# Kernel optimization log

Hardware: AMD Instinct MI355X
Metric: run time of the kernel (lower is better)

The kernel has to match this reference:

```python
import jax, jax.numpy as jnp
import numpy as np

E, H = 256, 4
DH = E // H                      # head dim 64
DHALF, N, R, K = 256, 16, 16, 5  # mamba d_inner//2, d_state, dt_rank, d_conv
B, L = 2, 2048


def _ln(x, g, b):
    m = jnp.mean(x, -1, keepdims=True)
    v = jnp.var(x, -1, keepdims=True)
    return (x - m) * jax.lax.rsqrt(v + 1e-5) * g + b


def _rotate_half(x):
    y = x.reshape(x.shape[:-1] + (-1, 2))
    return jnp.stack((-y[..., 1], y[..., 0]), -1).reshape(x.shape)


def _dwconv(x, w):  # x: (B,C,L), w: (C,1,K), depthwise 'same' conv, no bias (conv_bias//2 == 0)
    return jax.lax.conv_general_dilated(
        x, w, (1,), 'SAME', feature_group_count=x.shape[1],
        dimension_numbers=('NCH', 'OIH', 'NCH'))


def _selective_scan(x, dt, A_log, Bm, Cm, Dp, dt_bias):
    # x, dt: (B,Dh,L); Bm, Cm: (B,N,L); A_log: (Dh,N); Dp, dt_bias: (Dh,)
    A = -jnp.exp(A_log)
    delta = jax.nn.softplus(dt + dt_bias[None, :, None])
    seq = (jnp.moveaxis(delta, 2, 0), jnp.moveaxis(x, 2, 0),
           jnp.moveaxis(Bm, 2, 0), jnp.moveaxis(Cm, 2, 0))
    h0 = jnp.zeros((x.shape[0], A.shape[0], A.shape[1]), x.dtype)

    def step(h, inp):
        d_l, x_l, B_l, C_l = inp
        h = jnp.exp(d_l[:, :, None] * A) * h + (d_l * x_l)[:, :, None] * B_l[:, None, :]
        return h, jnp.einsum('bdn,bn->bd', h, C_l)

    _, ys = jax.lax.scan(step, h0, seq)
    return jnp.moveaxis(ys, 0, 2) + Dp[None, :, None] * x


def _forward(desc0, desc1, pe0, pe1, qkv_w, qkv_b, attn_out_w, attn_out_b,
             ma_ffn_w1, ma_ffn_b1, ma_ffn_g, ma_ffn_beta, ma_ffn_w2, ma_ffn_b2,
             m_in_w, m_convx_w, m_convz_w, m_xproj_w, m_dt_w, m_dt_b, m_Alog, m_D, m_out_w,
             ca_qk_w, ca_qk_b, ca_v_w, ca_v_b, ca_out_w, ca_out_b,
             ca_ffn_w1, ca_ffn_b1, ca_ffn_g, ca_ffn_beta, ca_ffn_w2, ca_ffn_b2):

    def mamba_twopath(x_in):
        xz = jnp.swapaxes(x_in @ m_in_w.T, 1, 2)           # (B, 2*Dh, L)
        xc, zc = xz[:, :DHALF], xz[:, DHALF:]
        xc = jax.nn.silu(_dwconv(xc, m_convx_w))
        zc = jax.nn.silu(_dwconv(zc, m_convz_w))
        x_dbl = jnp.einsum('bdl,kd->bkl', xc, m_xproj_w)   # (B, R+2N, L)
        # dt_proj applies its bias here AND the same bias is re-added inside the scan
        # (delta_bias), exactly as in the torch source.
        dt = jnp.einsum('brl,dr->bdl', x_dbl[:, :R], m_dt_w) + m_dt_b[None, :, None]
        Bm, Cm = x_dbl[:, R:R + N], x_dbl[:, R + N:]
        y = _selective_scan(xc, dt, m_Alog, Bm, Cm, m_D, m_dt_b)  # (B, Dh, L)
        return jnp.swapaxes(y, 1, 2) @ m_out_w.T, jnp.swapaxes(zc, 1, 2) @ m_out_w.T

    def ma_ffn(h):
        h = _ln(h @ ma_ffn_w1.T + ma_ffn_b1, ma_ffn_g, ma_ffn_beta)
        return jax.nn.gelu(h, approximate=False) @ ma_ffn_w2.T + ma_ffn_b2

    def mamba_attention(x, pe):
        b, l, _ = x.shape
        qkv = (x @ qkv_w.T + qkv_b).reshape(b, l, H, DH, 3)
        qkv = jnp.swapaxes(qkv, 1, 2)                       # (B,H,L,DH,3)
        q, k, v = qkv[..., 0], qkv[..., 1], qkv[..., 2]
        q = q * pe[0] + _rotate_half(q) * pe[1]
        k = k * pe[0] + _rotate_half(k) * pe[1]
        attn = jax.nn.softmax(jnp.einsum('bhid,bhjd->bhij', q, k) * DH ** -0.5, -1)
        o = jnp.einsum('bhij,bhjd->bhid', attn, v)
        o = jnp.swapaxes(o, 1, 2).reshape(b, l, E) @ attn_out_w.T + attn_out_b
        s_x, c_x = mamba_twopath(x)
        return x + ma_ffn(jnp.concatenate([x, o, s_x, c_x], -1))

    def ca_ffn(h):
        h = _ln(h @ ca_ffn_w1.T + ca_ffn_b1, ca_ffn_g, ca_ffn_beta)
        return jax.nn.gelu(h, approximate=False) @ ca_ffn_w2.T + ca_ffn_b2

    def split_heads(t):
        b, l, _ = t.shape
        return jnp.swapaxes(t.reshape(b, l, H, DH), 1, 2)

    def cross_attn(x0, x1):
        s = DH ** -0.25  # scale**0.5 applied to both qk0 and qk1
        qk0 = split_heads(x0 @ ca_qk_w.T + ca_qk_b) * s
        qk1 = split_heads(x1 @ ca_qk_w.T + ca_qk_b) * s
        v0 = split_heads(x0 @ ca_v_w.T + ca_v_b)
        v1 = split_heads(x1 @ ca_v_w.T + ca_v_b)
        sim = jnp.einsum('bhid,bhjd->bhij', qk0, qk1)       # (B,H,L0,L1)
        m0 = jnp.einsum('bhij,bhjd->bhid', jax.nn.softmax(sim, -1), v1)
        m1 = jnp.einsum('bhji,bhjd->bhid', jax.nn.softmax(sim, -2), v0)
        b, l = x0.shape[0], x0.shape[1]
        m0 = jnp.swapaxes(m0, 1, 2).reshape(b, l, E) @ ca_out_w.T + ca_out_b
        m1 = jnp.swapaxes(m1, 1, 2).reshape(b, x1.shape[1], E) @ ca_out_w.T + ca_out_b
        x0 = x0 + ca_ffn(jnp.concatenate([x0, m0], -1))
        x1 = x1 + ca_ffn(jnp.concatenate([x1, m1], -1))
        return x0, x1

    d0 = mamba_attention(desc0, pe0)
    d1 = mamba_attention(desc1, pe1)
    return cross_attn(d0, d1)


def setup_inputs():
    key = jax.random.key(0)
    ks = jax.random.split(key, 32)
    rn = lambda i, shape, s=0.02: jax.random.normal(ks[i], shape, jnp.float32) * s
    rng = np.random.default_rng(0)
    dt = np.exp(rng.uniform(size=DHALF) * (np.log(0.1) - np.log(0.001)) + np.log(0.001))
    inv_dt = dt + np.log(-np.expm1(-dt))
    return {
        'desc0': jax.random.normal(ks[0], (B, L, E), jnp.float32),
        'desc1': jax.random.normal(ks[1], (B, L, E), jnp.float32),
        'pe0': jax.random.normal(ks[2], (2, B, 1, L, DH), jnp.float32),
        'pe1': jax.random.normal(ks[3], (2, B, 1, L, DH), jnp.float32),
        'qkv_w': rn(4, (3 * E, E)), 'qkv_b': rn(5, (3 * E,)),
        'attn_out_w': rn(6, (E, E)), 'attn_out_b': rn(7, (E,)),
        'ma_ffn_w1': rn(8, (2 * E, 4 * E)), 'ma_ffn_b1': rn(9, (2 * E,)),
        'ma_ffn_g': jnp.ones((2 * E,), jnp.float32), 'ma_ffn_beta': jnp.zeros((2 * E,), jnp.float32),
        'ma_ffn_w2': rn(10, (E, 2 * E)), 'ma_ffn_b2': rn(11, (E,)),
        'm_in_w': rn(12, (2 * DHALF, E)),
        'm_convx_w': rn(13, (DHALF, 1, K), 0.2), 'm_convz_w': rn(14, (DHALF, 1, K), 0.2),
        'm_xproj_w': rn(15, (R + 2 * N, DHALF)),
        'm_dt_w': rn(16, (DHALF, R), R ** -0.5),
        'm_dt_b': jnp.asarray(inv_dt, jnp.float32),
        'm_Alog': jnp.log(jnp.broadcast_to(jnp.arange(1, N + 1, dtype=jnp.float32), (DHALF, N))),
        'm_D': jnp.ones((DHALF,), jnp.float32),
        'm_out_w': rn(17, (E, DHALF)),
        'ca_qk_w': rn(18, (E, E)), 'ca_qk_b': rn(19, (E,)),
        'ca_v_w': rn(20, (E, E)), 'ca_v_b': rn(21, (E,)),
        'ca_out_w': rn(22, (E, E)), 'ca_out_b': rn(23, (E,)),
        'ca_ffn_w1': rn(24, (2 * E, 2 * E)), 'ca_ffn_b1': rn(25, (2 * E,)),
        'ca_ffn_g': jnp.ones((2 * E,), jnp.float32), 'ca_ffn_beta': jnp.zeros((2 * E,), jnp.float32),
        'ca_ffn_w2': rn(26, (E, 2 * E)), 'ca_ffn_b2': rn(27, (E,)),
    }


def reference(desc0, desc1, pe0, pe1, qkv_w, qkv_b, attn_out_w, attn_out_b,
              ma_ffn_w1, ma_ffn_b1, ma_ffn_g, ma_ffn_beta, ma_ffn_w2, ma_ffn_b2,
              m_in_w, m_convx_w, m_convz_w, m_xproj_w, m_dt_w, m_dt_b, m_Alog, m_D, m_out_w,
              ca_qk_w, ca_qk_b, ca_v_w, ca_v_b, ca_out_w, ca_out_b,
              ca_ffn_w1, ca_ffn_b1, ca_ffn_g, ca_ffn_beta, ca_ffn_w2, ca_ffn_b2):
    return _forward(desc0, desc1, pe0, pe1, qkv_w, qkv_b, attn_out_w, attn_out_b,
                    ma_ffn_w1, ma_ffn_b1, ma_ffn_g, ma_ffn_beta, ma_ffn_w2, ma_ffn_b2,
                    m_in_w, m_convx_w, m_convz_w, m_xproj_w, m_dt_w, m_dt_b, m_Alog, m_D, m_out_w,
                    ca_qk_w, ca_qk_b, ca_v_w, ca_v_b, ca_out_w, ca_out_b,
                    ca_ffn_w1, ca_ffn_b1, ca_ffn_g, ca_ffn_beta, ca_ffn_w2, ca_ffn_b2)
```

## Files before the change

### kernel.cpp

```cpp
#include <hip/hip_runtime.h>

typedef unsigned short u16;
typedef short s16;
typedef s16 s16x8 __attribute__((ext_vector_type(8)));
typedef float f32x4 __attribute__((ext_vector_type(4)));

__device__ __forceinline__ float bf2f(u16 u){
  union { unsigned int i; float f; } v; v.i = ((unsigned int)u) << 16; return v.f;
}
__device__ __forceinline__ u16 f2bf(float f){
  union { float f; unsigned int u; } v; v.f = f;
  unsigned int r = (v.u + 0x7fffu + ((v.u >> 16) & 1u)) >> 16;
  return (u16)r;
}
__device__ __forceinline__ unsigned int cvtpk(float lo, float hi){
  unsigned int d;
  asm("v_cvt_pk_bf16_f32 %0, %1, %2" : "=v"(d) : "v"(lo), "v"(hi));
  return d;
}
__device__ __forceinline__ uint4 pack8(float4 a0, float4 a1){
  uint4 v;
  v.x = cvtpk(a0.x, a0.y); v.y = cvtpk(a0.z, a0.w);
  v.z = cvtpk(a1.x, a1.y); v.w = cvtpk(a1.z, a1.w);
  return v;
}
__device__ __forceinline__ float gelu_f(float x){
  return 0.5f * x * (1.f + erff(x * 0.70710678118654752440f));
}
__device__ __forceinline__ float ldw(const void* p, long i, int fl){
  return fl ? bf2f(((const u16*)p)[i]) : ((const float*)p)[i];
}
__device__ __forceinline__ float4 ldw4(const void* p, long i, int fl){
  if (fl){
    ushort4 w = *(const ushort4*)((const u16*)p + i);
    return make_float4(bf2f(w.x), bf2f(w.y), bf2f(w.z), bf2f(w.w));
  }
  return *(const float4*)((const float*)p + i);
}

template<int C>
__device__ __forceinline__ float dppf(float x){
  return __int_as_float(__builtin_amdgcn_update_dpp(0, __float_as_int(x), C, 0xf, 0xf, true));
}
__device__ __forceinline__ float dppmax16(float v){
  v = fmaxf(v, dppf<0xB1>(v));
  v = fmaxf(v, dppf<0x4E>(v));
  v = fmaxf(v, dppf<0x141>(v));
  v = fmaxf(v, dppf<0x140>(v));
  return v;
}
__device__ __forceinline__ float dppsum16(float v){
  v += dppf<0xB1>(v);
  v += dppf<0x4E>(v);
  v += dppf<0x141>(v);
  v += dppf<0x140>(v);
  return v;
}

__global__ __launch_bounds__(256) void k_sniff(const unsigned int* __restrict__ w,
                                               int n, int* __restrict__ flag){
  __shared__ int cnt[256];
  int c = 0;
  for (int i = threadIdx.x; i < n; i += 256){
    unsigned e = (w[i] >> 7) & 0xFFu;
    c += (e >= 120u && e <= 127u) ? 1 : 0;
  }
  cnt[threadIdx.x] = c; __syncthreads();
  for (int s = 128; s > 0; s >>= 1){
    if (threadIdx.x < s) cnt[threadIdx.x] += cnt[threadIdx.x + s];
    __syncthreads();
  }
  if (threadIdx.x == 0) flag[0] = (2 * cnt[0] > n) ? 1 : 0;
  if (threadIdx.x == 1) flag[1] = 0;
}

__global__ __launch_bounds__(256) void k_pad(
  const void* __restrict__ wx, const void* __restrict__ wd,
  const void* __restrict__ bd,
  float* __restrict__ px, float* __restrict__ pd, float* __restrict__ pb,
  const int* __restrict__ flagp)
{
  int fl = *flagp;
  int i = blockIdx.x * 256 + threadIdx.x;
  if (i < 16384){
    int r = i >> 8, c = i & 255;
    px[i] = (r < 48) ? ldw(wx, r*256 + c, fl) : 0.f;
  } else if (i < 32768){
    int j = i - 16384;
    int n = j >> 6, k = j & 63;
    pd[j] = (k < 16) ? ldw(wd, n*16 + k, fl) : 0.f;
  } else if (i < 33024){
    pb[i - 32768] = ldw(bd, i - 32768, fl);
  }
}

__global__ __launch_bounds__(256) void k_gemm_mfma(
  const void* __restrict__ A, int aflidx, int lda, int K, int N,
  const void* __restrict__ W, const void* __restrict__ W2, int nsplit, int wflidx,
  const void* __restrict__ bias,
  float* __restrict__ Cf, u16* __restrict__ Cb, int ldc,
  float* __restrict__ C2, int ldc2,
  const void* __restrict__ resid, int rflidx, int ldr,
  const void* __restrict__ csrc, int cflidx, float* __restrict__ cdst,
  float oscale, int act_gelu, int outmode, const int* __restrict__ flagp)
{
  const int fl  = flagp[0];
  const int afl = flagp[aflidx];
  const int wfl = flagp[wflidx];
  const int rfl = flagp[rflidx];
  const int cfl = flagp[cflidx];
  __shared__ u16 As[64*72];
  __shared__ u16 Bs[64*72];
  const int tid = threadIdx.x;
  const int w = tid >> 6, lane = tid & 63, quad = lane >> 4, m = lane & 15;
  const int m0 = blockIdx.y << 6, n0 = blockIdx.x << 6;
  const int srow = tid >> 2, sc0 = (tid & 3) << 4;
  const int reg2 = (n0 >= nsplit);
  const void* Wp = reg2 ? W2 : W;
  const int nbase = reg2 ? nsplit : 0;

  f32x4 acc[4];
  #pragma unroll
  for (int ct = 0; ct < 4; ++ct) acc[ct] = (f32x4){0.f,0.f,0.f,0.f};

  for (int k0 = 0; k0 < K; k0 += 64){
    {
      long ab = (long)(m0 + srow) * lda + k0 + sc0;
      if (afl && !act_gelu){
        #pragma unroll
        for (int g = 0; g < 2; ++g)
          *(uint4*)&As[srow*72 + sc0 + g*8] = *(const uint4*)((const u16*)A + ab + g*8);
      } else {
        #pragma unroll
        for (int g = 0; g < 2; ++g){
          float4 a0 = ldw4(A, ab + g*8, afl);
          float4 a1 = ldw4(A, ab + g*8 + 4, afl);
          if (act_gelu){
            a0.x=gelu_f(a0.x); a0.y=gelu_f(a0.y); a0.z=gelu_f(a0.z); a0.w=gelu_f(a0.w);
            a1.x=gelu_f(a1.x); a1.y=gelu_f(a1.y); a1.z=gelu_f(a1.z); a1.w=gelu_f(a1.w);
          }
          *(uint4*)&As[srow*72 + sc0 + g*8] = pack8(a0, a1);
        }
      }
    }
    {
      long wb = (long)(n0 + srow - nbase) * K + k0 + sc0;
      if (wfl){
        #pragma unroll
        for (int g = 0; g < 2; ++g)
          *(uint4*)&Bs[srow*72 + sc0 + g*8] = *(const uint4*)((const u16*)Wp + wb + g*8);
      } else {
        #pragma unroll
        for (int g = 0; g < 2; ++g){
          float4 b0 = *(const float4*)((const float*)Wp + wb + g*8);
          float4 b1 = *(const float4*)((const float*)Wp + wb + g*8 + 4);
          *(uint4*)&Bs[srow*72 + sc0 + g*8] = pack8(b0, b1);
        }
      }
    }
    __syncthreads();

    s16x8 av[2];
    #pragma unroll
    for (int s = 0; s < 2; ++s)
      av[s] = *(const s16x8*)&As[(w*16 + m)*72 + s*32 + quad*8];
    #pragma unroll
    for (int ct = 0; ct < 4; ++ct)
      #pragma unroll
      for (int s = 0; s < 2; ++s){
        s16x8 bv = *(const s16x8*)&Bs[(ct*16 + m)*72 + s*32 + quad*8];
        acc[ct] = __builtin_amdgcn_mfma_f32_16x16x32_bf16(av[s], bv, acc[ct], 0, 0, 0);
      }
    __syncthreads();
  }

  if (outmode == 4){
    const int gmb = m0 + w*16 + quad*4;
    #pragma unroll
    for (int ct = 0; ct < 4; ++ct){
      int gn = n0 + ct*16 + m;
      float bv = ldw(bias, gn, wfl);
      float dl4[4], dx4[4];
      #pragma unroll
      for (int r = 0; r < 4; ++r){
        float dl = acc[ct][r] + bv + bv;
        float delta = (dl > 20.f) ? dl : __logf(1.f + __expf(dl));
        dl4[r] = delta;
        dx4[r] = delta * ldw(resid, (long)(gmb + r) * ldr + gn, rfl);
      }
      *(float4*)&Cf[(long)gn * ldc + gmb] = make_float4(dl4[0], dl4[1], dl4[2], dl4[3]);
      *(float4*)&C2[(long)gn * ldc2 + gmb] = make_float4(dx4[0], dx4[1], dx4[2], dx4[3]);
    }
    return;
  }

  #pragma unroll
  for (int r = 0; r < 4; ++r){
    int gm = m0 + w*16 + quad*4 + r;
    #pragma unroll
    for (int ct = 0; ct < 4; ++ct){
      int gn = n0 + ct*16 + m;
      float v = acc[ct][r];
      if (reg2){
        C2[(long)gm * ldc2 + (gn - nsplit)] = v;
      } else {
        if (bias) v += ldw(bias, gn, wfl);
        v *= oscale;
        if (resid) v += ldw(resid, (long)gm * ldr + gn, rfl);
        long off = (long)gm * ldc + gn;
        if (outmode == 2){
          if (fl) Cb[off] = f2bf(v); else Cf[off] = v;
        } else if (outmode == 3){
          Cb[off] = f2bf(v);
        } else {
          Cf[off] = v;
        }
        if (cdst) cdst[(long)gm * ldc + gn] = ldw(csrc, (long)gm * 256 + gn, cfl);
      }
    }
  }
}

struct GB8 {
  const float* A[8]; const void* W[8]; const void* bias[8];
  float* Cf[8]; u16* Cb[8]; const void* resid[8];
  const void* csrc[8]; float* cdst[8]; float osc[8];
  int cfl[8]; int wkoff[8]; int rfli[8];
  const float* aux[8]; const void* dvec;
};

__global__ __launch_bounds__(256) void k_gemmb(
  GB8 gb, int lda, int K, int N, int ldc, int ldr, int ldwq,
  int act_gelu, int outmode, const int* __restrict__ flagp)
{
  const int fl = flagp[0];
  const int z = blockIdx.z;
  const float* A = gb.A[z]; const void* W = gb.W[z]; const void* bias = gb.bias[z];
  float* Cf = gb.Cf[z]; u16* Cb = gb.Cb[z]; const void* resid = gb.resid[z];
  const void* csrc = gb.csrc[z]; float* cdst = gb.cdst[z];
  const float osc = gb.osc[z];
  const int cfl = flagp[gb.cfl[z]];
  const int rfl = flagp[gb.rfli[z]];
  const int wkoff = gb.wkoff[z];
  const float* aux = gb.aux[z];

  __shared__ u16 As[64*72];
  __shared__ u16 Bs[64*72];
  const int tid = threadIdx.x;
  const int w = tid >> 6, lane = tid & 63, quad = lane >> 4, m = lane & 15;
  const int m0 = blockIdx.y << 6, n0 = blockIdx.x << 6;
  const int srow = tid >> 2, sc0 = (tid & 3) << 4;

  f32x4 acc[4];
  #pragma unroll
  for (int ct = 0; ct < 4; ++ct) acc[ct] = (f32x4){0.f,0.f,0.f,0.f};

  for (int k0 = 0; k0 < K; k0 += 64){
    {
      const float* ar = A + (long)(m0 + srow) * lda + k0 + sc0;
      #pragma unroll
      for (int g = 0; g < 2; ++g){
        float4 a0 = *(const float4*)(ar + g*8);
        float4 a1 = *(const float4*)(ar + g*8 + 4);
        if (aux){
          const float* xr = aux + (long)(m0 + srow) * lda + k0 + sc0;
          float4 x0 = *(const float4*)(xr + g*8);
          float4 x1 = *(const float4*)(xr + g*8 + 4);
          float4 d0 = ldw4(gb.dvec, k0 + sc0 + g*8, fl);
          float4 d1 = ldw4(gb.dvec, k0 + sc0 + g*8 + 4, fl);
          a0.x += d0.x*x0.x; a0.y += d0.y*x0.y; a0.z += d0.z*x0.z; a0.w += d0.w*x0.w;
          a1.x += d1.x*x1.x; a1.y += d1.y*x1.y; a1.z += d1.z*x1.z; a1.w += d1.w*x1.w;
        }
        if (act_gelu){
          a0.x=gelu_f(a0.x); a0.y=gelu_f(a0.y); a0.z=gelu_f(a0.z); a0.w=gelu_f(a0.w);
          a1.x=gelu_f(a1.x); a1.y=gelu_f(a1.y); a1.z=gelu_f(a1.z); a1.w=gelu_f(a1.w);
        }
        *(uint4*)&As[srow*72 + sc0 + g*8] = pack8(a0, a1);
      }
    }
    {
      long wb = (long)(n0 + srow) * ldwq + wkoff + k0 + sc0;
      if (fl){
        #pragma unroll
        for (int g = 0; g < 2; ++g)
          *(uint4*)&Bs[srow*72 + sc0 + g*8] = *(const uint4*)((const u16*)W + wb + g*8);
      } else {
        #pragma unroll
        for (int g = 0; g < 2; ++g){
          float4 b0 = *(const float4*)((const float*)W + wb + g*8);
          float4 b1 = *(const float4*)((const float*)W + wb + g*8 + 4);
          *(uint4*)&Bs[srow*72 + sc0 + g*8] = pack8(b0, b1);
        }
      }
    }
    __syncthreads();

    s16x8 av[2];
    #pragma unroll
    for (int s = 0; s < 2; ++s)
      av[s] = *(const s16x8*)&As[(w*16 + m)*72 + s*32 + quad*8];
    #pragma unroll
    for (int ct = 0; ct < 4; ++ct)
      #pragma unroll
      for (int s = 0; s < 2; ++s){
        s16x8 bv = *(const s16x8*)&Bs[(ct*16 + m)*72 + s*32 + quad*8];
        acc[ct] = __builtin_amdgcn_mfma_f32_16x16x32_bf16(av[s], bv, acc[ct], 0, 0, 0);
      }
    __syncthreads();
  }

  #pragma unroll
  for (int r = 0; r < 4; ++r){
    int gm = m0 + w*16 + quad*4 + r;
    #pragma unroll
    for (int ct = 0; ct < 4; ++ct){
      int gn = n0 + ct*16 + m;
      float v = acc[ct][r];
      if (bias) v += ldw(bias, gn, fl);
      v *= osc;
      if (resid) v += ldw(resid, (long)gm * ldr + gn, rfl);
      long off = (long)gm * ldc + gn;
      if (outmode == 2){
        if (fl) Cb[off] = f2bf(v); else Cf[off] = v;
      } else if (outmode == 3){
        Cb[off] = f2bf(v);
      } else {
        Cf[off] = v;
      }
      if (cdst) cdst[(long)gm * ldc + gn] = ldw(csrc, (long)gm * 256 + gn, cfl);
    }
  }
}

__global__ __launch_bounds__(256) void k_rope(
  const float* __restrict__ qkv0, const float* __restrict__ qkv1,
  const void* __restrict__ pe0, const void* __restrict__ pe1,
  u16* __restrict__ q, u16* __restrict__ k, u16* __restrict__ v,
  int L, int B, int H, const int* __restrict__ flagp)
{
  int fl = *flagp;
  int tid = threadIdx.x;
  int lq = tid >> 6, d = tid & 63;
  int l = blockIdx.x * 4 + lq;
  int bh = blockIdx.y;
  int dsc = bh >> 3;
  int bh7 = bh & 7;
  int b = bh7 >> 2, h = bh7 & 3;
  const float* qkv = dsc ? qkv1 : qkv0;
  const void* pe = dsc ? pe1 : pe0;
  const float* row = qkv + ((long)b * L + l) * 768 + h * 192;
  float qv = row[d*3+0], kv = row[d*3+1], vv = row[d*3+2];
  int dn = (d & 1) ? (d - 1) : (d + 1);
  float qn = row[dn*3+0], kn = row[dn*3+1];
  float rq = (d & 1) ? qn : -qn;
  float rk = (d & 1) ? kn : -kn;
  long peo = ((long)b * L + l) * 64 + d;
  float p0 = ldw(pe, peo, fl);
  float p1 = ldw(pe, (long)B * L * 64 + peo, fl);
  long o = ((long)bh * L + l) * 64 + d;
  q[o] = f2bf((qv * p0 + rq * p1) * 0.125f);
  k[o] = f2bf(kv * p0 + rk * p1);
  v[o] = f2bf(vv);
}

__global__ __launch_bounds__(256, 8) void k_attn_mfma(
  const u16* __restrict__ Q, long qsb, long qsh, long qsl,
  const u16* __restrict__ Kp, long ksb, long ksh, long ksl,
  const u16* __restrict__ Vp, long vsb, long vsh, long vsl,
  float* __restrict__ Opart, float* __restrict__ mpart, float* __restrict__ lpart,
  int L, int H, int kchunk)
{
  __shared__ u16 Kt[64*72];
  __shared__ u16 Vt[64*72];
  __shared__ u16 Ps[64*72];
  const int tid  = threadIdx.x;
  const int w    = tid >> 6;
  const int lane = tid & 63;
  const int quad = lane >> 4;
  const int m    = lane & 15;
  const int bh = blockIdx.y, b = bh / H, h = bh % H;
  const int iq0 = blockIdx.x * 64;
  const int z = blockIdx.z;
  const long BHL = (long)gridDim.y * L;

  const u16* Qb = Q  + b*qsb + h*qsh;
  const u16* Kb = Kp + b*ksb + h*ksh;
  const u16* Vb = Vp + b*vsb + h*vsh;

  s16x8 aq[2];
  {
    const u16* qr = Qb + (long)(iq0 + w*16 + m) * qsl + quad*8;
    aq[0] = *(const s16x8*)(qr);
    aq[1] = *(const s16x8*)(qr + 32);
  }

  f32x4 o_acc[4];
  #pragma unroll
  for (int nt = 0; nt < 4; ++nt) o_acc[nt] = (f32x4){0.f,0.f,0.f,0.f};
  float mrow[4] = {-1e30f,-1e30f,-1e30f,-1e30f};
  float lrow[4] = {0.f,0.f,0.f,0.f};

  const int srow = tid >> 2, sc0 = (tid & 3) << 4;
  const int kg = tid & 15;
  const int dg = tid >> 4;
  const int vcb = ((((dg >> 2) * 2) + (kg >> 1)) & 7) * 8 + (kg & 1) * 4;
  const int modd = m & 1;
  const int pcolb = m & 6;
  const int jend = z * kchunk + kchunk;

  for (int j0 = z * kchunk; j0 < jend; j0 += 64){
    {
      const u16* kr = Kb + (long)(j0 + srow) * ksl + sc0;
      *(uint4*)&Kt[srow*72 + sc0]     = *(const uint4*)kr;
      *(uint4*)&Kt[srow*72 + sc0 + 8] = *(const uint4*)(kr + 8);
      const u16* vr = Vb + (long)(j0 + 4*kg) * vsl + 4*dg;
      ushort4 r0 = *(const ushort4*)(vr);
      ushort4 r1 = *(const ushort4*)(vr + vsl);
      ushort4 r2 = *(const ushort4*)(vr + 2*vsl);
      ushort4 r3 = *(const ushort4*)(vr + 3*vsl);
      u16* vt = &Vt[(4*dg)*72 + vcb];
      *(ushort4*)(vt)       = make_ushort4(r0.x, r1.x, r2.x, r3.x);
      *(ushort4*)(vt + 72)  = make_ushort4(r0.y, r1.y, r2.y, r3.y);
      *(ushort4*)(vt + 144) = make_ushort4(r0.z, r1.z, r2.z, r3.z);
      *(ushort4*)(vt + 216) = make_ushort4(r0.w, r1.w, r2.w, r3.w);
    }
    __syncthreads();

    float sv[4][4];
    #pragma unroll
    for (int ct = 0; ct < 4; ++ct){
      f32x4 acc = (f32x4){0.f,0.f,0.f,0.f};
      #pragma unroll
      for (int s = 0; s < 2; ++s){
        s16x8 bk = *(const s16x8*)&Kt[(ct*16 + m)*72 + s*32 + quad*8];
        acc = __builtin_amdgcn_mfma_f32_16x16x32_bf16(aq[s], bk, acc, 0, 0, 0);
      }
      #pragma unroll
      for (int r = 0; r < 4; ++r) sv[ct][r] = acc[r];
    }

    float v0s[4];
    int need = 0;
    #pragma unroll
    for (int r = 0; r < 4; ++r){
      float v0 = fmaxf(fmaxf(sv[0][r], sv[1][r]), fmaxf(sv[2][r], sv[3][r]));
      v0 = dppmax16(v0);
      v0s[r] = v0;
      need |= (v0 > mrow[r] + 8.f) ? 1 : 0;
    }
    if (__any(need)){
      float alpha[4];
      #pragma unroll
      for (int r = 0; r < 4; ++r){
        float mn = fmaxf(mrow[r], v0s[r]);
        alpha[r] = __expf(mrow[r] - mn);
        mrow[r] = mn;
        lrow[r] *= alpha[r];
      }
      #pragma unroll
      for (int nt = 0; nt < 4; ++nt)
        #pragma unroll
        for (int r = 0; r < 4; ++r) o_acc[nt][r] *= alpha[r];
    }
    float rsum[4] = {0.f,0.f,0.f,0.f};
    #pragma unroll
    for (int ct = 0; ct < 4; ++ct)
      #pragma unroll
      for (int r = 0; r < 4; ++r){
        float p = __expf(sv[ct][r] - mrow[r]);
        sv[ct][r] = p;
        rsum[r] += p;
      }
    #pragma unroll
    for (int r = 0; r < 4; ++r)
      lrow[r] += dppsum16(rsum[r]);

    #pragma unroll
    for (int ct = 0; ct < 4; ++ct){
      const int kb = (2*w + 2*ct + (m >> 3)) & 7;
      const int col = (kb << 3) | pcolb;
      #pragma unroll
      for (int rr = 0; rr < 2; ++rr){
        float nb_lo = dppf<0xB1>(sv[ct][rr]);
        float nb_hi = dppf<0xB1>(sv[ct][2+rr]);
        float lo = modd ? nb_hi       : sv[ct][rr];
        float hi = modd ? sv[ct][2+rr] : nb_lo;
        unsigned int pk = cvtpk(lo, hi);
        int row = w*16 + quad*4 + rr + 2*modd;
        *(unsigned int*)&Ps[row*72 + col] = pk;
      }
    }
    asm volatile("s_waitcnt lgkmcnt(0)" ::: "memory");

    s16x8 ap[2];
    #pragma unroll
    for (int s = 0; s < 2; ++s)
      ap[s] = *(const s16x8*)&Ps[(w*16 + m)*72 + (((2*w + 4*s + quad) & 7) << 3)];
    #pragma unroll
    for (int nt = 0; nt < 4; ++nt)
      #pragma unroll
      for (int s = 0; s < 2; ++s){
        s16x8 bv = *(const s16x8*)&Vt[(nt*16 + m)*72 + (((2*nt + 4*s + quad) & 7) << 3)];
        o_acc[nt] = __builtin_amdgcn_mfma_f32_16x16x32_bf16(ap[s], bv, o_acc[nt], 0, 0, 0);
      }
    __syncthreads();
  }

  const long zOoff = (long)z * BHL * 64;
  #pragma unroll
  for (int r = 0; r < 4; ++r){
    int iq = iq0 + w*16 + quad*4 + r;
    long rowid = ((long)b*L + iq) * H + h;
    #pragma unroll
    for (int nt = 0; nt < 4; ++nt)
      Opart[zOoff + rowid*64 + nt*16 + m] = o_acc[nt][r];
    if (m == 0){
      mpart[(long)z*BHL + rowid] = mrow[r];
      lpart[(long)z*BHL + rowid] = lrow[r];
    }
  }
}

__global__ __launch_bounds__(256) void k_attn_comb(
  const float* Opart, const float* mpart, const float* lpart,
  float* O, long BHL)
{
  long i = (long)blockIdx.x * 256 + threadIdx.x;
  long row = i >> 6;
  float mv[4];
  float M = -1e30f;
  #pragma unroll
  for (int z = 0; z < 4; ++z){
    mv[z] = mpart[(long)z*BHL + row];
    M = fmaxf(M, mv[z]);
  }
  long N64 = BHL * 64;
  float T = 0.f, acc = 0.f;
  #pragma unroll
  for (int z = 0; z < 4; ++z){
    float wz = __expf(mv[z] - M);
    T   += lpart[(long)z*BHL + row] * wz;
    acc += Opart[(long)z*N64 + i] * wz;
  }
  O[i] = acc / T;
}

__global__ __launch_bounds__(256) void k_conv2(
  const float* __restrict__ xz,
  const void* __restrict__ wx, const void* __restrict__ wz,
  float* __restrict__ outx, float* __restrict__ outz,
  int L, const int* __restrict__ flagp)
{
  int fl = *flagp;
  int c = threadIdx.x;
  int bl = blockIdx.x; int b = bl / L, l = bl % L;
  int choff = blockIdx.y ? 256 : 0;
  const void* w = blockIdx.y ? wz : wx;
  float* out = blockIdx.y ? outz : outx;
  const float* base = xz + ((long)b * L) * 512 + choff + c;
  float s = 0.f;
  #pragma unroll
  for (int kk = 0; kk < 5; ++kk){
    int ll = l + kk - 2;
    if (ll >= 0 && ll < L) s += base[(long)ll * 512] * ldw(w, c*5 + kk, fl);
  }
  out[((long)b * L + l) * 256 + c] = s / (1.f + __expf(-s));
}

#define SC_CS 64
#define SC_NC 32

__global__ __launch_bounds__(256) void k_scan1(
  const float* __restrict__ deltaT, const float* __restrict__ dxcT,
  const float* __restrict__ xdbl, const void* __restrict__ Alog,
  float* __restrict__ E_out, float* __restrict__ F_out,
  int L, int ldt, const int* __restrict__ flagp)
{
  int fl = *flagp;
  int tid = threadIdx.x;
  int g = tid >> 4, n = tid & 15;
  int gid = blockIdx.x * 16 + g;
  int chunk = gid & (SC_NC - 1);
  int p = gid >> 5;
  int b = p >> 8, d = p & 255;
  float A = -__expf(ldw(Alog, d*16 + n, fl));
  const float* dTp = deltaT + (long)d*ldt + (long)b*L;
  const float* dxp = dxcT  + (long)d*ldt + (long)b*L;
  const float* xdb = xdbl + (long)b*L*64;
  int l0 = chunk * SC_CS;
  float E = 1.f, F = 0.f;
  for (int i = 0; i < SC_CS; i += 4){
    int l = l0 + i;
    float4 dt4 = *(const float4*)(dTp + l);
    float4 dx4 = *(const float4*)(dxp + l);
    float e[4], u[4];
    e[0] = __expf(dt4.x * A); e[1] = __expf(dt4.y * A);
    e[2] = __expf(dt4.z * A); e[3] = __expf(dt4.w * A);
    u[0] = dx4.x * xdb[(l+0)*64 + 16 + n];
    u[1] = dx4.y * xdb[(l+1)*64 + 16 + n];
    u[2] = dx4.z * xdb[(l+2)*64 + 16 + n];
    u[3] = dx4.w * xdb[(l+3)*64 + 16 + n];
    F = e[0]*F + u[0]; F = e[1]*F + u[1];
    F = e[2]*F + u[2]; F = e[3]*F + u[3];
    E *= (e[0]*e[1]) * (e[2]*e[3]);
  }
  long idx = (long)(p*16 + n) * SC_NC + chunk;
  E_out[idx] = E; F_out[idx] = F;
}

__global__ __launch_bounds__(256) void k_scan2(
  const float* __restrict__ E, const float* __restrict__ F,
  float* __restrict__ Hin)
{
  int pn = blockIdx.x * 256 + threadIdx.x;
  const float* Ep = E + (long)pn * SC_NC;
  const float* Fp = F + (long)pn * SC_NC;
  float* Hp = Hin + (long)pn * SC_NC;
  float h = 0.f;
  #pragma unroll
  for (int c = 0; c < SC_NC; ++c){
    Hp[c] = h;
    h = Ep[c] * h + Fp[c];
  }
}

__global__ __launch_bounds__(256) void k_scan3(
  const float* __restrict__ deltaT, const float* __restrict__ dxcT,
  const float* __restrict__ xdbl, const void* __restrict__ Alog,
  const float* __restrict__ Hin, float* __restrict__ y,
  int L, int ldt, const int* __restrict__ flagp)
{
  int fl = *flagp;
  int tid = threadIdx.x;
  int g = tid >> 4, n = tid & 15;
  int gid = blockIdx.x * 16 + g;
  int chunk = gid & (SC_NC - 1);
  int p = gid >> 5;
  int b = p >> 8, d = p & 255;
  float A = -__expf(ldw(Alog, d*16 + n, fl));
  const float* dTp = deltaT + (long)d*ldt + (long)b*L;
  const float* dxp = dxcT  + (long)d*ldt + (long)b*L;
  const float* xdb = xdbl + (long)b*L*64;
  float* yb = y + (long)b*L*256 + d;
  long idx = (long)(p*16 + n) * SC_NC + chunk;
  float h = Hin[idx];
  int l0 = chunk * SC_CS;
  for (int i = 0; i < SC_CS; i += 4){
    int l = l0 + i;
    float4 dt4 = *(const float4*)(dTp + l);
    float4 dx4 = *(const float4*)(dxp + l);
    float e[4], u[4], cm[4];
    e[0] = __expf(dt4.x * A); e[1] = __expf(dt4.y * A);
    e[2] = __expf(dt4.z * A); e[3] = __expf(dt4.w * A);
    u[0] = dx4.x * xdb[(l+0)*64 + 16 + n];
    u[1] = dx4.y * xdb[(l+1)*64 + 16 + n];
    u[2] = dx4.z * xdb[(l+2)*64 + 16 + n];
    u[3] = dx4.w * xdb[(l+3)*64 + 16 + n];
    cm[0] = xdb[(l+0)*64 + 32 + n];
    cm[1] = xdb[(l+1)*64 + 32 + n];
    cm[2] = xdb[(l+2)*64 + 32 + n];
    cm[3] = xdb[(l+3)*64 + 32 + n];
    float s0, s1, s2, s3;
    h = e[0]*h + u[0]; s0 = h * cm[0];
    h = e[1]*h + u[1]; s1 = h * cm[1];
    h = e[2]*h + u[2]; s2 = h * cm[2];
    h = e[3]*h + u[3]; s3 = h * cm[3];
    s0 += __shfl_xor(s0, 1, 16); s1 += __shfl_xor(s1, 1, 16);
    s2 += __shfl_xor(s2, 1, 16); s3 += __shfl_xor(s3, 1, 16);
    s0 += __shfl_xor(s0, 2, 16); s1 += __shfl_xor(s1, 2, 16);
    s2 += __shfl_xor(s2, 2, 16); s3 += __shfl_xor(s3, 2, 16);
    s0 += __shfl_xor(s0, 4, 16); s1 += __shfl_xor(s1, 4, 16);
    s2 += __shfl_xor(s2, 4, 16); s3 += __shfl_xor(s3, 4, 16);
    s0 += __shfl_xor(s0, 8, 16); s1 += __shfl_xor(s1, 8, 16);
    s2 += __shfl_xor(s2, 8, 16); s3 += __shfl_xor(s3, 8, 16);
    if (n < 4){
      float out = (n == 0) ? s0 : (n == 1) ? s1 : (n == 2) ? s2 : s3;
      yb[(long)(l + n)*256] = out;
    }
  }
}

__global__ __launch_bounds__(256) void k_ln2(
  float* __restrict__ hA, const float* __restrict__ hA2,
  float* __restrict__ hB, const float* __restrict__ hB2,
  const void* __restrict__ g, const void* __restrict__ beta,
  const int* __restrict__ flagp)
{
  int fl = *flagp;
  int r = blockIdx.x * 4 + (threadIdx.x >> 6);
  float* hbase = (r < 4096) ? hA : hB;
  const float* h2base = (r < 4096) ? hA2 : hB2;
  int row = r & 4095;
  int lane = threadIdx.x & 63;
  float* hr = hbase + (long)row * 512;
  const float* h2r = h2base + (long)row * 512;
  float v[8]; float s = 0.f, ss = 0.f;
  #pragma unroll
  for (int i = 0; i < 8; ++i){
    v[i] = hr[lane + 64*i] + h2r[lane + 64*i];
    s += v[i]; ss += v[i]*v[i];
  }
  #pragma unroll
  for (int off = 1; off < 64; off <<= 1){ s += __shfl_xor(s, off); ss += __shfl_xor(ss, off); }
  float mean = s * (1.f/512.f);
  float var  = ss * (1.f/512.f) - mean * mean;
  float rs = rsqrtf(var + 1e-5f);
  #pragma unroll
  for (int i = 0; i < 8; ++i){
    int c = lane + 64*i;
    hr[c] = (v[i] - mean) * rs * ldw(g, c, fl) + ldw(beta, c, fl);
  }
}

extern "C" void kernel_launch(void* const* d_in, const int* in_sizes, int n_in,
                              void* d_out, int out_size, void* d_ws, size_t ws_size,
                              hipStream_t stream)
{
  const int B_ = 2, L_ = 2048, H_ = 4;
  const long BLE = (long)B_ * L_ * 256;
  const long BHLb = 2L * B_ * H_ * L_;
  const long BHLc = (long)B_ * H_ * L_;

  int* flagp = (int*)d_ws;
  float* base = (float*)d_ws + 64;

  float* cat0   = base + 0*BLE;
  float* cat1   = base + 3*BLE;
  float* xz01   = base + 6*BLE;
  u16*   q01    = (u16*)(base + 10*BLE);
  u16*   k01    = (u16*)(base + 11*BLE);
  u16*   v01    = (u16*)(base + 12*BLE);
  float* Opart  = base + 13*BLE;
  float* ob01   = base + 21*BLE;
  float* mml    = base + 23*BLE;
  float* mll    = mml + 4*32768;
  float* xc01   = base + 24*BLE;
  float* zc01   = base + 26*BLE;
  float* xdbl01 = base + 28*BLE;
  float* delta01= base + 29*BLE;
  float* dxc01  = base + 31*BLE;
  float* scE    = base + 33*BLE;
  float* scF    = scE + 524288;
  float* scH    = scF + 524288;
  float* y01    = base + 35*BLE;
  float* catc0  = base + 37*BLE;
  float* catc1  = base + 41*BLE;
  float* h0     = base + 45*BLE;
  float* part0  = base + 47*BLE;
  float* h1     = base + 49*BLE;
  float* part1  = base + 51*BLE;
  float* dbuf0  = base + 53*BLE;
  float* dbuf1  = base + 54*BLE;
  u16*   qc     = (u16*)(base + 55*BLE);
  u16*   kc     = qc + 1048576;
  u16*   vc     = kc + 1048576;
  u16*   oc     = vc + 1048576;
  float* catA   = base + 57*BLE;
  float* catB   = base + 59*BLE;
  float* px     = base + 61*BLE;
  float* pd     = px + 16384;
  float* pb     = pd + 16384;

  const void* in[35];
  for (int i = 0; i < 35 && i < n_in; ++i) in[i] = d_in[i];

  k_sniff<<<1, 256, 0, stream>>>((const unsigned int*)in[0], 2048, flagp);
  k_pad<<<130, 256, 0, stream>>>(in[17], in[18], in[19], px, pd, pb, flagp);

  const int BIG = 1 << 30;
  const long sbP = (long)H_ * L_ * 64, shP = (long)L_ * 64, slP = 64;
  const long sbF = (long)L_ * 256,     shF = 64,            slF = 256;
  const int kchunk = L_ / 4;
  const int MROWS = 4 * L_;

  k_gemm_mfma<<<dim3(20, 64), 256, 0, stream>>>(
      in[0], 0, 256, 256, 1280, in[4], in[14], 768, 0, in[5],
      cat0, nullptr, 768, xz01, 512,
      nullptr, 1, 0, nullptr, 1, nullptr, 1.f, 0, 0, flagp);
  k_gemm_mfma<<<dim3(20, 64), 256, 0, stream>>>(
      in[1], 0, 256, 256, 1280, in[4], in[14], 768, 0, in[5],
      cat1, nullptr, 768, xz01 + 2*BLE, 512,
      nullptr, 1, 0, nullptr, 1, nullptr, 1.f, 0, 0, flagp);
  k_rope<<<dim3(L_/4, 16), 256, 0, stream>>>(cat0, cat1, in[2], in[3],
      q01, k01, v01, L_, B_, H_, flagp);
  k_attn_mfma<<<dim3(L_/64, 16, 4), 256, 0, stream>>>(
      q01, sbP, shP, slP, k01, sbP, shP, slP, v01, sbP, shP, slP,
      Opart, mml, mll, L_, H_, kchunk);
  k_attn_comb<<<8192, 256, 0, stream>>>(Opart, mml, mll, ob01, BHLb);
  k_conv2<<<dim3(2*B_*L_, 2), 256, 0, stream>>>(xz01, in[15], in[16], xc01, zc01, L_, flagp);
  k_gemm_mfma<<<dim3(1, 128), 256, 0, stream>>>(
      xc01, 1, 256, 256, 64, px, nullptr, BIG, 1, nullptr,
      xdbl01, nullptr, 64, nullptr, 0,
      nullptr, 1, 0, nullptr, 1, nullptr, 1.f, 0, 0, flagp);
  k_gemm_mfma<<<dim3(4, 128), 256, 0, stream>>>(
      xdbl01, 1, 64, 64, 256, pd, nullptr, BIG, 1, pb,
      delta01, nullptr, MROWS, dxc01, MROWS,
      xc01, 1, 256, nullptr, 1, nullptr, 1.f, 0, 4, flagp);
  k_scan1<<<2048, 256, 0, stream>>>(delta01, dxc01, xdbl01, in[20], scE, scF, L_, MROWS, flagp);
  k_scan2<<<64, 256, 0, stream>>>(scE, scF, scH);
  k_scan3<<<2048, 256, 0, stream>>>(delta01, dxc01, xdbl01, in[20], scH, y01, L_, MROWS, flagp);
  {
    GB8 gb = {};
    gb.dvec = in[21];
    gb.A[0] = y01;        gb.aux[0] = xc01;       gb.W[0] = in[22]; gb.Cf[0] = catc0 + 512; gb.osc[0] = 1.f; gb.cfl[0] = 1;
    gb.A[1] = zc01;       gb.W[1] = in[22]; gb.Cf[1] = catc0 + 768; gb.osc[1] = 1.f; gb.cfl[1] = 1;
    gb.A[2] = ob01;       gb.W[2] = in[6];  gb.bias[2] = in[7];     gb.Cf[2] = catc0 + 256;
    gb.csrc[2] = in[0];   gb.cdst[2] = catc0; gb.osc[2] = 1.f;      gb.cfl[2] = 0;
    gb.A[3] = y01 + BLE;  gb.aux[3] = xc01 + BLE; gb.W[3] = in[22]; gb.Cf[3] = catc1 + 512; gb.osc[3] = 1.f; gb.cfl[3] = 1;
    gb.A[4] = zc01 + BLE; gb.W[4] = in[22]; gb.Cf[4] = catc1 + 768; gb.osc[4] = 1.f; gb.cfl[4] = 1;
    gb.A[5] = ob01 + BLE; gb.W[5] = in[6];  gb.bias[5] = in[7];     gb.Cf[5] = catc1 + 256;
    gb.csrc[5] = in[1];   gb.cdst[5] = catc1; gb.osc[5] = 1.f;      gb.cfl[5] = 0;
    k_gemmb<<<dim3(4, 64, 6), 256, 0, stream>>>(gb, 256, 256, 256, 1024, 0, 256, 0, 0, flagp);
  }
  {
    GB8 gb = {};
    gb.cfl[0] = gb.cfl[1] = gb.cfl[2] = gb.cfl[3] = 1;
    gb.A[0] = catc0;       gb.W[0] = in[8]; gb.bias[0] = in[9]; gb.Cf[0] = h0;    gb.osc[0] = 1.f;
    gb.A[1] = catc0 + 512; gb.W[1] = in[8]; gb.wkoff[1] = 512;  gb.Cf[1] = part0; gb.osc[1] = 1.f;
    gb.A[2] = catc1;       gb.W[2] = in[8]; gb.bias[2] = in[9]; gb.Cf[2] = h1;    gb.osc[2] = 1.f;
    gb.A[3] = catc1 + 512; gb.W[3] = in[8]; gb.wkoff[3] = 512;  gb.Cf[3] = part1; gb.osc[3] = 1.f;
    k_gemmb<<<dim3(8, 64, 4), 256, 0, stream>>>(gb, 1024, 512, 512, 512, 0, 1024, 0, 0, flagp);
  }
  k_ln2<<<2048, 256, 0, stream>>>(h0, part0, h1, part1, in[10], in[11], flagp);
  {
    GB8 gb = {};
    gb.cfl[0] = gb.cfl[1] = 1;
    gb.A[0] = h0; gb.W[0] = in[12]; gb.bias[0] = in[13]; gb.resid[0] = in[0]; gb.rfli[0] = 0;
    gb.Cf[0] = dbuf0; gb.osc[0] = 1.f;
    gb.A[1] = h1; gb.W[1] = in[12]; gb.bias[1] = in[13]; gb.resid[1] = in[1]; gb.rfli[1] = 0;
    gb.Cf[1] = dbuf1; gb.osc[1] = 1.f;
    k_gemmb<<<dim3(4, 64, 2), 256, 0, stream>>>(gb, 512, 512, 256, 256, 256, 512, 1, 0, flagp);
  }

  const float s4 = 0.35355339059327373f;
  float* cm0 = xc01;
  float* cm1 = xc01 + BLE;
  {
    GB8 gb = {};
    gb.cfl[0] = gb.cfl[1] = gb.cfl[2] = gb.cfl[3] = 1;
    gb.A[0] = dbuf0; gb.W[0] = in[23]; gb.bias[0] = in[24]; gb.Cb[0] = qc; gb.osc[0] = s4;
    gb.A[1] = dbuf1; gb.W[1] = in[23]; gb.bias[1] = in[24]; gb.Cb[1] = kc; gb.osc[1] = s4;
    gb.A[2] = dbuf0; gb.W[2] = in[25]; gb.bias[2] = in[26]; gb.Cb[2] = vc; gb.osc[2] = 1.f;
    gb.A[3] = dbuf1; gb.W[3] = in[25]; gb.bias[3] = in[26]; gb.Cb[3] = oc; gb.osc[3] = 1.f;
    k_gemmb<<<dim3(4, 64, 4), 256, 0, stream>>>(gb, 256, 256, 256, 256, 0, 256, 0, 3, flagp);
  }
  k_attn_mfma<<<dim3(L_/64, B_*H_, 4), 256, 0, stream>>>(
      qc, sbF, shF, slF, kc, sbF, shF, slF, oc, sbF, shF, slF,
      Opart, mml, mll, L_, H_, kchunk);
  k_attn_comb<<<4096, 256, 0, stream>>>(Opart, mml, mll, cm0, BHLc);
  k_attn_mfma<<<dim3(L_/64, B_*H_, 4), 256, 0, stream>>>(
      kc, sbF, shF, slF, qc, sbF, shF, slF, vc, sbF, shF, slF,
      Opart, mml, mll, L_, H_, kchunk);
  k_attn_comb<<<4096, 256, 0, stream>>>(Opart, mml, mll, cm1, BHLc);
  {
    GB8 gb = {};
    gb.cfl[0] = gb.cfl[1] = 1;
    gb.A[0] = cm0; gb.W[0] = in[27]; gb.bias[0] = in[28]; gb.Cf[0] = catA + 256;
    gb.csrc[0] = dbuf0; gb.cdst[0] = catA; gb.osc[0] = 1.f;
    gb.A[1] = cm1; gb.W[1] = in[27]; gb.bias[1] = in[28]; gb.Cf[1] = catB + 256;
    gb.csrc[1] = dbuf1; gb.cdst[1] = catB; gb.osc[1] = 1.f;
    k_gemmb<<<dim3(4, 64, 2), 256, 0, stream>>>(gb, 256, 256, 256, 512, 0, 256, 0, 0, flagp);
  }
  {
    GB8 gb = {};
    gb.cfl[0] = gb.cfl[1] = gb.cfl[2] = gb.cfl[3] = 1;
    gb.A[0] = catA;       gb.W[0] = in[29]; gb.bias[0] = in[30]; gb.Cf[0] = h0;    gb.osc[0] = 1.f;
    gb.A[1] = catA + 256; gb.W[1] = in[29]; gb.wkoff[1] = 256;   gb.Cf[1] = part0; gb.osc[1] = 1.f;
    gb.A[2] = catB;       gb.W[2] = in[29]; gb.bias[2] = in[30]; gb.Cf[2] = h1;    gb.osc[2] = 1.f;
    gb.A[3] = catB + 256; gb.W[3] = in[29]; gb.wkoff[3] = 256;   gb.Cf[3] = part1; gb.osc[3] = 1.f;
    k_gemmb<<<dim3(8, 64, 4), 256, 0, stream>>>(gb, 512, 256, 512, 512, 0, 512, 0, 0, flagp);
  }
  k_ln2<<<2048, 256, 0, stream>>>(h0, part0, h1, part1, in[31], in[32], flagp);
  {
    GB8 gb = {};
    gb.cfl[0] = gb.cfl[1] = 1;
    gb.rfli[0] = gb.rfli[1] = 1;
    gb.A[0] = h0; gb.W[0] = in[33]; gb.bias[0] = in[34]; gb.resid[0] = dbuf0;
    gb.Cf[0] = (float*)d_out; gb.Cb[0] = (u16*)d_out; gb.osc[0] = 1.f;
    gb.A[1] = h1; gb.W[1] = in[33]; gb.bias[1] = in[34]; gb.resid[1] = dbuf1;
    gb.Cf[1] = (float*)d_out + BLE; gb.Cb[1] = (u16*)d_out + BLE; gb.osc[1] = 1.f;
    k_gemmb<<<dim3(4, 64, 2), 256, 0, stream>>>(gb, 512, 512, 256, 256, 256, 512, 1, 2, flagp);
  }
}
```

Baseline: 657.8 us.

## Batch paired launches, use exp2 softmax with pre-scaled Q, halve attention key splits

The two input-projection GEMMs are merged into one launch over a z dimension, and the two cross-attention directions are merged into one launch using a batch-xor trick to pick the other descriptor's keys. Softmax switches from exp to exp2, with log2(e) folded into the Q scaling. The key-split count drops from 4 to 2, which halves the partial buffers and the combine work. The aim is fewer launches and cheaper exponentials. The trade-off is less parallelism per attention launch, and the merged cross-attention relies on a specific buffer layout that must line up.

Measured after the change: 657.4 us. No clear change (-0.1%).

```diff
diff --git a/kernel.cpp b/kernel.cpp
--- a/kernel.cpp
+++ b/kernel.cpp
@@ -95,20 +95,26 @@
 }
 
 __global__ __launch_bounds__(256) void k_gemm_mfma(
-  const void* __restrict__ A, int aflidx, int lda, int K, int N,
+  const void* __restrict__ A0, int aflidx, int lda, int K, int N,
   const void* __restrict__ W, const void* __restrict__ W2, int nsplit, int wflidx,
   const void* __restrict__ bias,
-  float* __restrict__ Cf, u16* __restrict__ Cb, int ldc,
-  float* __restrict__ C2, int ldc2,
+  float* __restrict__ Cf0, u16* __restrict__ Cb, int ldc,
+  float* __restrict__ C20, int ldc2,
   const void* __restrict__ resid, int rflidx, int ldr,
   const void* __restrict__ csrc, int cflidx, float* __restrict__ cdst,
-  float oscale, int act_gelu, int outmode, const int* __restrict__ flagp)
+  float oscale, int act_gelu, int outmode,
+  const void* __restrict__ A1, long coff1, long c2off1,
+  const int* __restrict__ flagp)
 {
   const int fl  = flagp[0];
   const int afl = flagp[aflidx];
   const int wfl = flagp[wflidx];
   const int rfl = flagp[rflidx];
   const int cfl = flagp[cflidx];
+  const void* A = A0;
+  float* Cf = Cf0;
+  float* C2 = C20;
+  if (blockIdx.z){ A = A1; Cf += coff1; C2 += c2off1; }
   __shared__ u16 As[64*72];
   __shared__ u16 Bs[64*72];
   const int tid = threadIdx.x;
@@ -358,7 +364,7 @@
   float p0 = ldw(pe, peo, fl);
   float p1 = ldw(pe, (long)B * L * 64 + peo, fl);
   long o = ((long)bh * L + l) * 64 + d;
-  q[o] = f2bf((qv * p0 + rq * p1) * 0.125f);
+  q[o] = f2bf((qv * p0 + rq * p1) * 0.18033688011112042f);
   k[o] = f2bf(kv * p0 + rk * p1);
   v[o] = f2bf(vv);
 }
@@ -368,7 +374,7 @@
   const u16* __restrict__ Kp, long ksb, long ksh, long ksl,
   const u16* __restrict__ Vp, long vsb, long vsh, long vsl,
   float* __restrict__ Opart, float* __restrict__ mpart, float* __restrict__ lpart,
-  int L, int H, int kchunk)
+  int L, int H, int kchunk, int bxor)
 {
   __shared__ u16 Kt[64*72];
   __shared__ u16 Vt[64*72];
@@ -383,9 +389,9 @@
   const int z = blockIdx.z;
   const long BHL = (long)gridDim.y * L;
 
-  const u16* Qb = Q  + b*qsb + h*qsh;
-  const u16* Kb = Kp + b*ksb + h*ksh;
-  const u16* Vb = Vp + b*vsb + h*vsh;
+  const u16* Qb = Q  + (long)b*qsb + h*qsh;
+  const u16* Kb = Kp + (long)(b^bxor)*ksb + h*ksh;
+  const u16* Vb = Vp + (long)(b^bxor)*vsb + h*vsh;
 
   s16x8 aq[2];
   {
@@ -453,7 +459,7 @@
       #pragma unroll
       for (int r = 0; r < 4; ++r){
         float mn = fmaxf(mrow[r], v0s[r]);
-        alpha[r] = __expf(mrow[r] - mn);
+        alpha[r] = exp2f(mrow[r] - mn);
         mrow[r] = mn;
         lrow[r] *= alpha[r];
       }
@@ -467,7 +473,7 @@
     for (int ct = 0; ct < 4; ++ct)
       #pragma unroll
       for (int r = 0; r < 4; ++r){
-        float p = __expf(sv[ct][r] - mrow[r]);
+        float p = exp2f(sv[ct][r] - mrow[r]);
         sv[ct][r] = p;
         rsum[r] += p;
       }
@@ -523,22 +529,20 @@
 
 __global__ __launch_bounds__(256) void k_attn_comb(
   const float* Opart, const float* mpart, const float* lpart,
-  float* O, long BHL)
+  float* O, long BHL, int nz)
 {
   long i = (long)blockIdx.x * 256 + threadIdx.x;
   long row = i >> 6;
   float mv[4];
   float M = -1e30f;
-  #pragma unroll
-  for (int z = 0; z < 4; ++z){
+  for (int z = 0; z < nz; ++z){
     mv[z] = mpart[(long)z*BHL + row];
     M = fmaxf(M, mv[z]);
   }
   long N64 = BHL * 64;
   float T = 0.f, acc = 0.f;
-  #pragma unroll
-  for (int z = 0; z < 4; ++z){
-    float wz = __expf(mv[z] - M);
+  for (int z = 0; z < nz; ++z){
+    float wz = exp2f(mv[z] - M);
     T   += lpart[(long)z*BHL + row] * wz;
     acc += Opart[(long)z*N64 + i] * wz;
   }
@@ -719,7 +723,6 @@
   const int B_ = 2, L_ = 2048, H_ = 4;
   const long BLE = (long)B_ * L_ * 256;
   const long BHLb = 2L * B_ * H_ * L_;
-  const long BHLc = (long)B_ * H_ * L_;
 
   int* flagp = (int*)d_ws;
   float* base = (float*)d_ws + 64;
@@ -733,7 +736,7 @@
   float* Opart  = base + 13*BLE;
   float* ob01   = base + 21*BLE;
   float* mml    = base + 23*BLE;
-  float* mll    = mml + 4*32768;
+  float* mll    = mml + 2*32768;
   float* xc01   = base + 24*BLE;
   float* zc01   = base + 26*BLE;
   float* xdbl01 = base + 28*BLE;
@@ -770,32 +773,33 @@
   const int BIG = 1 << 30;
   const long sbP = (long)H_ * L_ * 64, shP = (long)L_ * 64, slP = 64;
   const long sbF = (long)L_ * 256,     shF = 64,            slF = 256;
-  const int kchunk = L_ / 4;
+  const int NZ = 2;
+  const int kchunk = L_ / NZ;
   const int MROWS = 4 * L_;
-
-  k_gemm_mfma<<<dim3(20, 64), 256, 0, stream>>>(
+  const float LOG2E = 1.4426950408889634f;
+
+  k_gemm_mfma<<<dim3(20, 64, 2), 256, 0, stream>>>(
       in[0], 0, 256, 256, 1280, in[4], in[14], 768, 0, in[5],
       cat0, nullptr, 768, xz01, 512,
-      nullptr, 1, 0, nullptr, 1, nullptr, 1.f, 0, 0, flagp);
-  k_gemm_mfma<<<dim3(20, 64), 256, 0, stream>>>(
-      in[1], 0, 256, 256, 1280, in[4], in[14], 768, 0, in[5],
-      cat1, nullptr, 768, xz01 + 2*BLE, 512,
-      nullptr, 1, 0, nullptr, 1, nullptr, 1.f, 0, 0, flagp);
+      nullptr, 1, 0, nullptr, 1, nullptr, 1.f, 0, 0,
+      in[1], 3*BLE, 2*BLE, flagp);
   k_rope<<<dim3(L_/4, 16), 256, 0, stream>>>(cat0, cat1, in[2], in[3],
       q01, k01, v01, L_, B_, H_, flagp);
-  k_attn_mfma<<<dim3(L_/64, 16, 4), 256, 0, stream>>>(
+  k_attn_mfma<<<dim3(L_/64, 16, NZ), 256, 0, stream>>>(
       q01, sbP, shP, slP, k01, sbP, shP, slP, v01, sbP, shP, slP,
-      Opart, mml, mll, L_, H_, kchunk);
-  k_attn_comb<<<8192, 256, 0, stream>>>(Opart, mml, mll, ob01, BHLb);
+      Opart, mml, mll, L_, H_, kchunk, 0);
+  k_attn_comb<<<8192, 256, 0, stream>>>(Opart, mml, mll, ob01, BHLb, NZ);
   k_conv2<<<dim3(2*B_*L_, 2), 256, 0, stream>>>(xz01, in[15], in[16], xc01, zc01, L_, flagp);
   k_gemm_mfma<<<dim3(1, 128), 256, 0, stream>>>(
       xc01, 1, 256, 256, 64, px, nullptr, BIG, 1, nullptr,
       xdbl01, nullptr, 64, nullptr, 0,
-      nullptr, 1, 0, nullptr, 1, nullptr, 1.f, 0, 0, flagp);
+      nullptr, 1, 0, nullptr, 1, nullptr, 1.f, 0, 0,
+      nullptr, 0, 0, flagp);
   k_gemm_mfma<<<dim3(4, 128), 256, 0, stream>>>(
       xdbl01, 1, 64, 64, 256, pd, nullptr, BIG, 1, pb,
       delta01, nullptr, MROWS, dxc01, MROWS,
-      xc01, 1, 256, nullptr, 1, nullptr, 1.f, 0, 4, flagp);
+      xc01, 1, 256, nullptr, 1, nullptr, 1.f, 0, 4,
+      nullptr, 0, 0, flagp);
   k_scan1<<<2048, 256, 0, stream>>>(delta01, dxc01, xdbl01, in[20], scE, scF, L_, MROWS, flagp);
   k_scan2<<<64, 256, 0, stream>>>(scE, scF, scH);
   k_scan3<<<2048, 256, 0, stream>>>(delta01, dxc01, xdbl01, in[20], scH, y01, L_, MROWS, flagp);
@@ -834,31 +838,26 @@
 
   const float s4 = 0.35355339059327373f;
   float* cm0 = xc01;
-  float* cm1 = xc01 + BLE;
   {
     GB8 gb = {};
     gb.cfl[0] = gb.cfl[1] = gb.cfl[2] = gb.cfl[3] = 1;
-    gb.A[0] = dbuf0; gb.W[0] = in[23]; gb.bias[0] = in[24]; gb.Cb[0] = qc; gb.osc[0] = s4;
+    gb.A[0] = dbuf0; gb.W[0] = in[23]; gb.bias[0] = in[24]; gb.Cb[0] = qc; gb.osc[0] = s4 * LOG2E;
     gb.A[1] = dbuf1; gb.W[1] = in[23]; gb.bias[1] = in[24]; gb.Cb[1] = kc; gb.osc[1] = s4;
     gb.A[2] = dbuf0; gb.W[2] = in[25]; gb.bias[2] = in[26]; gb.Cb[2] = vc; gb.osc[2] = 1.f;
     gb.A[3] = dbuf1; gb.W[3] = in[25]; gb.bias[3] = in[26]; gb.Cb[3] = oc; gb.osc[3] = 1.f;
     k_gemmb<<<dim3(4, 64, 4), 256, 0, stream>>>(gb, 256, 256, 256, 256, 0, 256, 0, 3, flagp);
   }
-  k_attn_mfma<<<dim3(L_/64, B_*H_, 4), 256, 0, stream>>>(
-      qc, sbF, shF, slF, kc, sbF, shF, slF, oc, sbF, shF, slF,
-      Opart, mml, mll, L_, H_, kchunk);
-  k_attn_comb<<<4096, 256, 0, stream>>>(Opart, mml, mll, cm0, BHLc);
-  k_attn_mfma<<<dim3(L_/64, B_*H_, 4), 256, 0, stream>>>(
-      kc, sbF, shF, slF, qc, sbF, shF, slF, vc, sbF, shF, slF,
-      Opart, mml, mll, L_, H_, kchunk);
-  k_attn_comb<<<4096, 256, 0, stream>>>(Opart, mml, mll, cm1, BHLc);
+  k_attn_mfma<<<dim3(L_/64, 16, NZ), 256, 0, stream>>>(
+      qc, sbF, shF, slF, qc, sbF, shF, slF, vc, sbF, shF, slF,
+      Opart, mml, mll, L_, H_, kchunk, 2);
+  k_attn_comb<<<8192, 256, 0, stream>>>(Opart, mml, mll, cm0, BHLb, NZ);
   {
     GB8 gb = {};
     gb.cfl[0] = gb.cfl[1] = 1;
-    gb.A[0] = cm0; gb.W[0] = in[27]; gb.bias[0] = in[28]; gb.Cf[0] = catA + 256;
-    gb.csrc[0] = dbuf0; gb.cdst[0] = catA; gb.osc[0] = 1.f;
-    gb.A[1] = cm1; gb.W[1] = in[27]; gb.bias[1] = in[28]; gb.Cf[1] = catB + 256;
-    gb.csrc[1] = dbuf1; gb.cdst[1] = catB; gb.osc[1] = 1.f;
+    gb.A[0] = cm0;       gb.W[0] = in[27]; gb.bias[0] = in[28]; gb.Cf[0] = catA + 256;
+    gb.csrc[0] = dbuf0;  gb.cdst[0] = catA; gb.osc[0] = 1.f;
+    gb.A[1] = cm0 + BLE; gb.W[1] = in[27]; gb.bias[1] = in[28]; gb.Cf[1] = catB + 256;
+    gb.csrc[1] = dbuf1;  gb.cdst[1] = catB; gb.osc[1] = 1.f;
     k_gemmb<<<dim3(4, 64, 2), 256, 0, stream>>>(gb, 256, 256, 256, 512, 0, 256, 0, 0, flagp);
   }
   {
```
